# Performance work log

Hardware: AMD Instinct MI355X
Metric: run time of the kernel (lower is better)

The kernel has to match this reference:

```python
import jax, jax.numpy as jnp
import numpy as np

L, B, E, H = 4096, 4, 1024, 16
HD = E // H
EPS = 1e-4


def setup_inputs() -> dict:
    key = jax.random.key(0)
    ks = jax.random.split(key, 9)
    s = 1.0 / np.sqrt(E)
    return {
        "query": jax.random.normal(ks[0], (L, B, E), jnp.float32),
        "key_": jax.random.normal(ks[1], (L, B, E), jnp.float32),
        "value": jax.random.normal(ks[2], (L, B, E), jnp.float32),
        "Wq": jax.random.normal(ks[3], (E, E), jnp.float32) * s,
        "bq": jnp.zeros((E,), jnp.float32),
        "Wk": jax.random.normal(ks[4], (E, E), jnp.float32) * s,
        "bk": jnp.zeros((E,), jnp.float32),
        "Wv": jax.random.normal(ks[5], (E, E), jnp.float32) * s,
        "bv": jnp.zeros((E,), jnp.float32),
    }


def _heads(x):
    # (L, B, E) -> (B*H, L, HD)
    l = x.shape[0]
    return x.reshape(l, B * H, HD).transpose(1, 0, 2)


def reference(query, key_, value, Wq, bq, Wk, bk, Wv, bv):
    tgt_len = query.shape[0]
    src_len = key_.shape[0]
    q = _heads(query @ Wq.T + bq)
    k = _heads(key_ @ Wk.T + bk)
    v = _heads(value @ Wv.T + bv)
    # relu feature map (use_relu=True, constant=0)
    q = jax.nn.relu(q)
    k = jax.nn.relu(k)
    m = max(src_len, tgt_len)
    # pi/2 * arange(1, m+1) / m
    ang = (jnp.pi / 2) * jnp.arange(1, m + 1, dtype=q.dtype) / m  # (m,)
    sin = jnp.sin(ang)[None, :, None]
    cos = jnp.cos(ang)[None, :, None]
    q_ = jnp.concatenate([q * sin[:, :tgt_len], q * cos[:, :tgt_len]], axis=-1)  # (n, L, 2HD)
    k_ = jnp.concatenate([k * sin[:, :src_len], k * cos[:, :src_len]], axis=-1)
    # non-causal linear attention
    kv_ = jnp.einsum('nld,nlm->ndm', k_, v)                       # (n, 2HD, HD)
    z_ = 1.0 / jnp.maximum(jnp.einsum('nld,nd->nl', q_, k_.sum(axis=1)), EPS)
    attn = jnp.einsum('nld,ndm,nl->nlm', q_, kv_, z_)             # (n, L, HD)
    out = attn.transpose(1, 0, 2).reshape(tgt_len, B, E)
    return out
```

## Files before the change

### kernel.cpp

```cpp
#include <hip/hip_runtime.h>
#include <hip/hip_bf16.h>


typedef unsigned short ushortt;
typedef unsigned int u32;
typedef __attribute__((ext_vector_type(8))) short bf16x8;
typedef __attribute__((ext_vector_type(4))) float f32x4;

#define L_DIM 4096
#define B_DIM 4
#define E_DIM 1024

#define KV_CH 8
#define KV_LCH (L_DIM / KV_CH)
#define KV_LT 32

__device__ __forceinline__ ushortt f2bf(float f) {
    union { float f; u32 u; } v; v.f = f;
    u32 u = v.u;
    u += 0x7FFFu + ((u >> 16) & 1u);
    return (ushortt)(u >> 16);
}
__device__ __forceinline__ float bf2f(ushortt h) {
    union { u32 u; float f; } v; v.u = ((u32)h) << 16;
    return v.f;
}

__device__ __forceinline__ void gl_lds16(const void* g, void* l) {
    __builtin_amdgcn_global_load_lds(
        (const __attribute__((address_space(1))) unsigned int*)g,
        (__attribute__((address_space(3))) unsigned int*)l, 16, 0, 0);
}

__global__ __launch_bounds__(256) void k_cvtW(
    const float* __restrict__ W, ushortt* __restrict__ Wb)
{
    const int i = (blockIdx.x * 256 + threadIdx.x) * 4;
    const float4 v = *reinterpret_cast<const float4*>(W + i);
    ushortt o[4] = { f2bf(v.x), f2bf(v.y), f2bf(v.z), f2bf(v.w) };
    *reinterpret_cast<uint2*>(Wb + i) = *reinterpret_cast<uint2*>(o);
}

__global__ __launch_bounds__(256) void k_cvtX(
    const float* __restrict__ X, ushortt* __restrict__ Xb)
{
    const int i = (blockIdx.x * 256 + threadIdx.x) * 4;
    const float4 v = *reinterpret_cast<const float4*>(X + i);
    ushortt o[4] = { f2bf(v.x), f2bf(v.y), f2bf(v.z), f2bf(v.w) };
    *reinterpret_cast<uint2*>(Xb + i) = *reinterpret_cast<uint2*>(o);
}

__global__ __launch_bounds__(256) void k_gemmB(
    const ushortt* __restrict__ Xb, const ushortt* __restrict__ Wb,
    const float* __restrict__ bias,
    float* __restrict__ Of, ushortt* __restrict__ Ob, const int p)
{
    __shared__ char sA[2][8192];
    __shared__ char sB[2][8192];

    const int t = threadIdx.x;
    const int ln = t & 63;
    const int wv = t >> 6;
    const int wr = wv >> 1, wc = wv & 1;

    const int orig = blockIdx.x;
    const int bid = (orig & 7) * 128 + (orig >> 3);
    const int mblk = (bid >> 3) * 128;
    const int nblk = (bid & 7) * 128;

    f32x4 acc[4][4];
#pragma unroll
    for (int i = 0; i < 4; i++)
#pragma unroll
        for (int j = 0; j < 4; j++) acc[i][j] = (f32x4){0.f, 0.f, 0.f, 0.f};

    const int rowIn = ln >> 2;
    const int srcE  = ((ln & 3) ^ ((ln >> 3) & 3)) << 3;

    const int g   = ln >> 4;
    const int r15 = ln & 15;
    const int sw  = ((r15 >> 1) & 3) << 4;

    auto stage = [&](int buf, int k0) {
#pragma unroll
        for (int c = 0; c < 2; c++) {
            const int ch = wv * 2 + c;
            const int row = ch * 16 + rowIn;
            gl_lds16(Xb + (size_t)(mblk + row) * E_DIM + k0 + srcE, &sA[buf][ch * 1024]);
            gl_lds16(Wb + (size_t)(nblk + row) * E_DIM + k0 + srcE, &sB[buf][ch * 1024]);
        }
    };

    stage(0, 0);
    stage(1, 32);

    for (int tt = 0; tt < 32; tt++) {
        const int cur = tt & 1;
        if (tt < 31) {
            asm volatile("s_waitcnt vmcnt(4)" ::: "memory");
        } else {
            asm volatile("s_waitcnt vmcnt(0)" ::: "memory");
        }
        __builtin_amdgcn_sched_barrier(0);
        __builtin_amdgcn_s_barrier();

        bf16x8 va[4], vb[4];
#pragma unroll
        for (int i = 0; i < 4; i++) {
            const int row = wr * 64 + i * 16 + r15;
            va[i] = *reinterpret_cast<const bf16x8*>(&sA[cur][row * 64 + ((g * 16) ^ sw)]);
        }
#pragma unroll
        for (int j = 0; j < 4; j++) {
            const int n = wc * 64 + j * 16 + r15;
            vb[j] = *reinterpret_cast<const bf16x8*>(&sB[cur][n * 64 + ((g * 16) ^ sw)]);
        }
#pragma unroll
        for (int i = 0; i < 4; i++)
#pragma unroll
            for (int j = 0; j < 4; j++)
                acc[i][j] = __builtin_amdgcn_mfma_f32_16x16x32_bf16(va[i], vb[j], acc[i][j], 0, 0, 0);

        asm volatile("s_waitcnt lgkmcnt(0)" ::: "memory");
        __builtin_amdgcn_sched_barrier(0);
        __builtin_amdgcn_s_barrier();
        __builtin_amdgcn_sched_barrier(0);

        if (tt + 2 < 32) stage(cur, (tt + 2) * 32);
    }

#pragma unroll
    for (int j = 0; j < 4; j++) {
        const int col = nblk + wc * 64 + j * 16 + r15;
        const float bj = bias[col];
#pragma unroll
        for (int i = 0; i < 4; i++) {
            const int row0 = mblk + wr * 64 + i * 16 + g * 4;
#pragma unroll
            for (int r = 0; r < 4; r++) {
                float v = acc[i][j][r] + bj;
                if (p < 2) v = fmaxf(v, 0.0f);
                if (p == 0) Of[(size_t)(row0 + r) * E_DIM + col] = v;
                else        Ob[(size_t)(row0 + r) * E_DIM + col] = f2bf(v);
            }
        }
    }
}

__global__ __launch_bounds__(256) void k_kv3(
    const ushortt* __restrict__ Kb, const ushortt* __restrict__ Vb,
    float* __restrict__ pm, float* __restrict__ pd)
{
    __shared__ float sk[KV_LT][128];
    __shared__ float sv[KV_LT][64];

    const int head = blockIdx.x;
    const int b = head >> 4, hh = head & 15;
    const int t = threadIdx.x;
    const int mq = t & 7;
    const int dq = t >> 3;
    const int l0base = blockIdx.y * KV_LCH;

    float acc[4][8];
    float ksum[4];
#pragma unroll
    for (int i = 0; i < 4; i++) {
        ksum[i] = 0.0f;
#pragma unroll
        for (int j = 0; j < 8; j++) acc[i][j] = 0.0f;
    }

    const size_t headoff = (size_t)hh * 64;

    for (int l0 = l0base; l0 < l0base + KV_LCH; l0 += KV_LT) {
        __syncthreads();
#pragma unroll
        for (int i = 0; i < 2; i++) {
            const int j = t + 256 * i;
            const int l = j >> 4;
            const int c4 = (j & 15) << 2;
            const size_t rowb = ((size_t)(l0 + l) * B_DIM + b) * E_DIM + headoff;
            const uint2 kraw = *reinterpret_cast<const uint2*>(Kb + rowb + c4);
            const uint2 vraw = *reinterpret_cast<const uint2*>(Vb + rowb + c4);
            const float ang = 1.5707963267948966f * (float)(l0 + l + 1) * (1.0f / 4096.0f);
            const float sn = sinf(ang), cs = cosf(ang);
            const float k0 = bf2f((ushortt)(kraw.x & 0xffffu));
            const float k1 = bf2f((ushortt)(kraw.x >> 16));
            const float k2 = bf2f((ushortt)(kraw.y & 0xffffu));
            const float k3 = bf2f((ushortt)(kraw.y >> 16));
            *reinterpret_cast<float4*>(&sk[l][c4]) =
                make_float4(sn * k0, sn * k1, sn * k2, sn * k3);
            *reinterpret_cast<float4*>(&sk[l][64 + c4]) =
                make_float4(cs * k0, cs * k1, cs * k2, cs * k3);
            *reinterpret_cast<float4*>(&sv[l][c4]) =
                make_float4(bf2f((ushortt)(vraw.x & 0xffffu)),
                            bf2f((ushortt)(vraw.x >> 16)),
                            bf2f((ushortt)(vraw.y & 0xffffu)),
                            bf2f((ushortt)(vraw.y >> 16)));
        }
        __syncthreads();
#pragma unroll 8
        for (int l = 0; l < KV_LT; l++) {
            const float4 a4 = *reinterpret_cast<const float4*>(&sk[l][dq << 2]);
            const float4 v0 = *reinterpret_cast<const float4*>(&sv[l][mq << 3]);
            const float4 v1 = *reinterpret_cast<const float4*>(&sv[l][(mq << 3) + 4]);
            const float av[4] = { a4.x, a4.y, a4.z, a4.w };
            const float vv[8] = { v0.x, v0.y, v0.z, v0.w, v1.x, v1.y, v1.z, v1.w };
#pragma unroll
            for (int i = 0; i < 4; i++) {
#pragma unroll
                for (int j = 0; j < 8; j++) acc[i][j] += av[i] * vv[j];
                ksum[i] += av[i];
            }
        }
    }

    float* dstm = pm + ((size_t)blockIdx.y * 64 + head) * 8192;
    float* dstd = pd + ((size_t)blockIdx.y * 64 + head) * 128;
    const int d0 = dq << 2, m0 = mq << 3;
#pragma unroll
    for (int i = 0; i < 4; i++) {
        *reinterpret_cast<float4*>(&dstm[(d0 + i) * 64 + m0]) =
            make_float4(acc[i][0], acc[i][1], acc[i][2], acc[i][3]);
        *reinterpret_cast<float4*>(&dstm[(d0 + i) * 64 + m0 + 4]) =
            make_float4(acc[i][4], acc[i][5], acc[i][6], acc[i][7]);
        if (mq == 0) dstd[d0 + i] = ksum[i];
    }
}

__global__ __launch_bounds__(256) void k_kvred(
    const float* __restrict__ pm, const float* __restrict__ pd,
    float* __restrict__ kvm, float* __restrict__ kvd)
{
    const int bid = blockIdx.x, t = threadIdx.x;
    if (bid < 512) {
        const int g = bid * 256 + t;
        const int head = g >> 11, r = g & 2047;
        float4 s = make_float4(0.f, 0.f, 0.f, 0.f);
#pragma unroll
        for (int c = 0; c < KV_CH; c++) {
            const float4 v = reinterpret_cast<const float4*>(pm)[((size_t)(c * 64 + head) << 11) + r];
            s.x += v.x; s.y += v.y; s.z += v.z; s.w += v.w;
        }
        reinterpret_cast<float4*>(kvm)[g] = s;
    } else {
#pragma unroll
        for (int it = 0; it < 8; it++) {
            const int idx = it * 256 + t;
            const int head = idx >> 5, r = idx & 31;
            float4 s = make_float4(0.f, 0.f, 0.f, 0.f);
#pragma unroll
            for (int c = 0; c < KV_CH; c++) {
                const float4 v = reinterpret_cast<const float4*>(pd)[((size_t)(c * 64 + head) << 5) + r];
                s.x += v.x; s.y += v.y; s.z += v.z; s.w += v.w;
            }
            reinterpret_cast<float4*>(kvd)[idx] = s;
        }
    }
}

__global__ __launch_bounds__(256) void k_attn3(
    float* qout, const float* __restrict__ kvm, const float* __restrict__ kvd)
{
    __shared__ float skv[128][64];
    __shared__ float skd[128];
    __shared__ float sq[64][132];

    const int t = threadIdx.x;
    const int head = blockIdx.x;
    const int b = head >> 4, hh = head & 15;
    const int l0 = blockIdx.y * 64;

    const float* kvh = kvm + (size_t)head * (128 * 64);

#pragma unroll
    for (int c = 0; c < 8; c++) {
        const int idx = t + 256 * c;
        const int d = idx >> 4, m4 = (idx & 15) << 2;
        *reinterpret_cast<float4*>(&skv[d][m4]) =
            *reinterpret_cast<const float4*>(kvh + d * 64 + m4);
    }
    if (t < 128) skd[t] = kvd[(size_t)head * 128 + t];

    const size_t qbase = ((size_t)l0 * B_DIM + b) * E_DIM + (size_t)hh * 64;
#pragma unroll
    for (int c = 0; c < 4; c++) {
        const int idx = t + 256 * c;
        const int l = idx >> 4, q4 = (idx & 15) << 2;
        const float4 v = *reinterpret_cast<const float4*>(
            qout + qbase + (size_t)l * (B_DIM * E_DIM) + q4);
        const float ang = 1.5707963267948966f * (float)(l0 + l + 1) * (1.0f / 4096.0f);
        const float sn = sinf(ang), cs = cosf(ang);
        *reinterpret_cast<float4*>(&sq[l][q4]) =
            make_float4(sn * v.x, sn * v.y, sn * v.z, sn * v.w);
        *reinterpret_cast<float4*>(&sq[l][64 + q4]) =
            make_float4(cs * v.x, cs * v.y, cs * v.z, cs * v.w);
    }
    __syncthreads();

    const int tx = t & 15, ty = t >> 4;
    const int r = ty * 4, m0 = tx * 4;

    float4 acc[4];
    float accd[4];
#pragma unroll
    for (int i = 0; i < 4; i++) {
        acc[i] = make_float4(0.f, 0.f, 0.f, 0.f);
        accd[i] = 0.f;
    }

#pragma unroll 4
    for (int d0 = 0; d0 < 128; d0 += 4) {
        const float4 kd4 = *reinterpret_cast<const float4*>(&skd[d0]);
        float4 qv[4];
#pragma unroll
        for (int i = 0; i < 4; i++)
            qv[i] = *reinterpret_cast<const float4*>(&sq[r + i][d0]);
#pragma unroll
        for (int dd = 0; dd < 4; dd++) {
            const float4 kvv = *reinterpret_cast<const float4*>(&skv[d0 + dd][m0]);
            const float kdv = (dd == 0) ? kd4.x : (dd == 1) ? kd4.y : (dd == 2) ? kd4.z : kd4.w;
#pragma unroll
            for (int i = 0; i < 4; i++) {
                const float qs = (dd == 0) ? qv[i].x : (dd == 1) ? qv[i].y
                               : (dd == 2) ? qv[i].z : qv[i].w;
                acc[i].x += qs * kvv.x;
                acc[i].y += qs * kvv.y;
                acc[i].z += qs * kvv.z;
                acc[i].w += qs * kvv.w;
                accd[i] += qs * kdv;
            }
        }
    }

#pragma unroll
    for (int i = 0; i < 4; i++) {
        const float z = 1.0f / fmaxf(accd[i], 1e-4f);
        float4 vo = make_float4(acc[i].x * z, acc[i].y * z, acc[i].z * z, acc[i].w * z);
        *reinterpret_cast<float4*>(
            qout + qbase + (size_t)(r + i) * (B_DIM * E_DIM) + m0) = vo;
    }
}

extern "C" void kernel_launch(void* const* d_in, const int* in_sizes, int n_in,
                              void* d_out, int out_size, void* d_ws, size_t ws_size,
                              hipStream_t stream) {
    (void)in_sizes; (void)n_in; (void)out_size; (void)ws_size;
    const float* xq = (const float*)d_in[0];
    const float* xk = (const float*)d_in[1];
    const float* xv = (const float*)d_in[2];
    const float* wq = (const float*)d_in[3];
    const float* bq = (const float*)d_in[4];
    const float* wk = (const float*)d_in[5];
    const float* bk = (const float*)d_in[6];
    const float* wv = (const float*)d_in[7];
    const float* bv = (const float*)d_in[8];
    float* out = (float*)d_out;

    char* ws = (char*)d_ws;
    ushortt* Kb  = (ushortt*)(ws);
    ushortt* Vb  = (ushortt*)(ws + 33554432);
    ushortt* Wb  = (ushortt*)(ws + 67108864);
    float*   kvm = (float*)(ws + 67108864);
    float*   kvd = (float*)(ws + 67108864 + 2097152);
    ushortt* Xqb = (ushortt*)(ws);
    ushortt* Wqb = (ushortt*)(ws + 33554432);

    ushortt* Xkb = (ushortt*)d_out;
    ushortt* Xvb = (ushortt*)((char*)d_out + 33554432);
    float*   pm  = (float*)d_out;
    float*   pd  = (float*)((char*)d_out + 16777216);

    dim3 blk(256);
    k_cvtW<<<dim3(1024), blk, 0, stream>>>(wk, Wb);
    k_cvtX<<<dim3(16384), blk, 0, stream>>>(xk, Xkb);
    k_gemmB<<<dim3(1024), blk, 0, stream>>>(Xkb, Wb, bk, (float*)nullptr, Kb, 1);
    k_cvtW<<<dim3(1024), blk, 0, stream>>>(wv, Wb);
    k_cvtX<<<dim3(16384), blk, 0, stream>>>(xv, Xvb);
    k_gemmB<<<dim3(1024), blk, 0, stream>>>(Xvb, Wb, bv, (float*)nullptr, Vb, 2);
    k_kv3<<<dim3(64, KV_CH), blk, 0, stream>>>(Kb, Vb, pm, pd);
    k_kvred<<<dim3(513), blk, 0, stream>>>(pm, pd, kvm, kvd);
    k_cvtW<<<dim3(1024), blk, 0, stream>>>(wq, Wqb);
    k_cvtX<<<dim3(16384), blk, 0, stream>>>(xq, Xqb);
    k_gemmB<<<dim3(1024), blk, 0, stream>>>(Xqb, Wqb, bq, out, (ushortt*)nullptr, 0);
    k_attn3<<<dim3(64, 64), blk, 0, stream>>>(out, kvm, kvd);
}
```

Measured before the change: 557.0 us.

## Enlarge projection GEMM tiles to 256x256 with 512 threads and K-step 64

Replaces the 128x128-tile, 256-thread bf16 MFMA GEMM with a 256x256-tile, 512-thread version that stages K in chunks of 64 and uses a new XOR swizzle for the 128-byte LDS rows. It also hoists the bias loads ahead of the main loop. Larger tiles raise arithmetic intensity and halve the K-loop barrier count, which should cut global and LDS traffic per FLOP. The costs are 128 KB of LDS per block, more accumulator registers, and only 256 blocks, which may underfill the GPU's compute units.

```diff
diff --git a/kernel.cpp b/kernel.cpp
--- a/kernel.cpp
+++ b/kernel.cpp
@@ -50,95 +50,103 @@
     *reinterpret_cast<uint2*>(Xb + i) = *reinterpret_cast<uint2*>(o);
 }
 
-__global__ __launch_bounds__(256) void k_gemmB(
+__global__ __launch_bounds__(512, 2) void k_gemm256(
     const ushortt* __restrict__ Xb, const ushortt* __restrict__ Wb,
     const float* __restrict__ bias,
     float* __restrict__ Of, ushortt* __restrict__ Ob, const int p)
 {
-    __shared__ char sA[2][8192];
-    __shared__ char sB[2][8192];
+    __shared__ __align__(16) char sA[2][32768];
+    __shared__ __align__(16) char sB[2][32768];
 
     const int t = threadIdx.x;
     const int ln = t & 63;
     const int wv = t >> 6;
-    const int wr = wv >> 1, wc = wv & 1;
+    const int wr = wv >> 2;
+    const int wc = wv & 3;
 
     const int orig = blockIdx.x;
-    const int bid = (orig & 7) * 128 + (orig >> 3);
-    const int mblk = (bid >> 3) * 128;
-    const int nblk = (bid & 7) * 128;
-
-    f32x4 acc[4][4];
-#pragma unroll
-    for (int i = 0; i < 4; i++)
+    const int bid = (orig & 7) * 32 + (orig >> 3);
+    const int mblk = (bid >> 2) * 256;
+    const int nblk = (bid & 3) * 256;
+
+    f32x4 acc[8][4];
+#pragma unroll
+    for (int i = 0; i < 8; i++)
 #pragma unroll
         for (int j = 0; j < 4; j++) acc[i][j] = (f32x4){0.f, 0.f, 0.f, 0.f};
 
-    const int rowIn = ln >> 2;
-    const int srcE  = ((ln & 3) ^ ((ln >> 3) & 3)) << 3;
+    const int rowIn = ln >> 3;
+    const int srcE  = ((ln & 7) ^ rowIn) << 3;
 
     const int g   = ln >> 4;
     const int r15 = ln & 15;
-    const int sw  = ((r15 >> 1) & 3) << 4;
+    const int sw3 = r15 & 7;
 
     auto stage = [&](int buf, int k0) {
 #pragma unroll
-        for (int c = 0; c < 2; c++) {
-            const int ch = wv * 2 + c;
-            const int row = ch * 16 + rowIn;
+        for (int c = 0; c < 4; c++) {
+            const int ch = wv * 4 + c;
+            const int row = ch * 8 + rowIn;
             gl_lds16(Xb + (size_t)(mblk + row) * E_DIM + k0 + srcE, &sA[buf][ch * 1024]);
             gl_lds16(Wb + (size_t)(nblk + row) * E_DIM + k0 + srcE, &sB[buf][ch * 1024]);
         }
     };
 
+    float bj[4];
+#pragma unroll
+    for (int j = 0; j < 4; j++)
+        bj[j] = bias[nblk + wc * 64 + j * 16 + r15];
+    __builtin_amdgcn_sched_barrier(0);
+
     stage(0, 0);
-    stage(1, 32);
-
-    for (int tt = 0; tt < 32; tt++) {
+    stage(1, 64);
+
+    for (int tt = 0; tt < 16; tt++) {
         const int cur = tt & 1;
-        if (tt < 31) {
-            asm volatile("s_waitcnt vmcnt(4)" ::: "memory");
+        if (tt < 15) {
+            asm volatile("s_waitcnt vmcnt(8)" ::: "memory");
         } else {
             asm volatile("s_waitcnt vmcnt(0)" ::: "memory");
         }
         __builtin_amdgcn_sched_barrier(0);
         __builtin_amdgcn_s_barrier();
 
-        bf16x8 va[4], vb[4];
-#pragma unroll
-        for (int i = 0; i < 4; i++) {
-            const int row = wr * 64 + i * 16 + r15;
-            va[i] = *reinterpret_cast<const bf16x8*>(&sA[cur][row * 64 + ((g * 16) ^ sw)]);
-        }
-#pragma unroll
-        for (int j = 0; j < 4; j++) {
-            const int n = wc * 64 + j * 16 + r15;
-            vb[j] = *reinterpret_cast<const bf16x8*>(&sB[cur][n * 64 + ((g * 16) ^ sw)]);
-        }
-#pragma unroll
-        for (int i = 0; i < 4; i++)
-#pragma unroll
-            for (int j = 0; j < 4; j++)
-                acc[i][j] = __builtin_amdgcn_mfma_f32_16x16x32_bf16(va[i], vb[j], acc[i][j], 0, 0, 0);
+#pragma unroll
+        for (int ks = 0; ks < 2; ks++) {
+            const int off = ((ks * 4 + g) ^ sw3) << 4;
+            bf16x8 vb[4];
+#pragma unroll
+            for (int j = 0; j < 4; j++) {
+                const int row = wc * 64 + j * 16 + r15;
+                vb[j] = *reinterpret_cast<const bf16x8*>(&sB[cur][row * 128 + off]);
+            }
+#pragma unroll
+            for (int i = 0; i < 8; i++) {
+                const int row = wr * 128 + i * 16 + r15;
+                bf16x8 va = *reinterpret_cast<const bf16x8*>(&sA[cur][row * 128 + off]);
+#pragma unroll
+                for (int j = 0; j < 4; j++)
+                    acc[i][j] = __builtin_amdgcn_mfma_f32_16x16x32_bf16(va, vb[j], acc[i][j], 0, 0, 0);
+            }
+        }
 
         asm volatile("s_waitcnt lgkmcnt(0)" ::: "memory");
         __builtin_amdgcn_sched_barrier(0);
         __builtin_amdgcn_s_barrier();
         __builtin_amdgcn_sched_barrier(0);
 
-        if (tt + 2 < 32) stage(cur, (tt + 2) * 32);
+        if (tt + 2 < 16) stage(cur, (tt + 2) * 64);
     }
 
 #pragma unroll
     for (int j = 0; j < 4; j++) {
         const int col = nblk + wc * 64 + j * 16 + r15;
-        const float bj = bias[col];
-#pragma unroll
-        for (int i = 0; i < 4; i++) {
-            const int row0 = mblk + wr * 64 + i * 16 + g * 4;
+#pragma unroll
+        for (int i = 0; i < 8; i++) {
+            const int row0 = mblk + wr * 128 + i * 16 + g * 4;
 #pragma unroll
             for (int r = 0; r < 4; r++) {
-                float v = acc[i][j][r] + bj;
+                float v = acc[i][j][r] + bj[j];
                 if (p < 2) v = fmaxf(v, 0.0f);
                 if (p == 0) Of[(size_t)(row0 + r) * E_DIM + col] = v;
                 else        Ob[(size_t)(row0 + r) * E_DIM + col] = f2bf(v);
@@ -374,14 +382,14 @@
     dim3 blk(256);
     k_cvtW<<<dim3(1024), blk, 0, stream>>>(wk, Wb);
     k_cvtX<<<dim3(16384), blk, 0, stream>>>(xk, Xkb);
-    k_gemmB<<<dim3(1024), blk, 0, stream>>>(Xkb, Wb, bk, (float*)nullptr, Kb, 1);
+    k_gemm256<<<dim3(256), dim3(512), 0, stream>>>(Xkb, Wb, bk, (float*)nullptr, Kb, 1);
     k_cvtW<<<dim3(1024), blk, 0, stream>>>(wv, Wb);
     k_cvtX<<<dim3(16384), blk, 0, stream>>>(xv, Xvb);
-    k_gemmB<<<dim3(1024), blk, 0, stream>>>(Xvb, Wb, bv, (float*)nullptr, Vb, 2);
+    k_gemm256<<<dim3(256), dim3(512), 0, stream>>>(Xvb, Wb, bv, (float*)nullptr, Vb, 2);
     k_kv3<<<dim3(64, KV_CH), blk, 0, stream>>>(Kb, Vb, pm, pd);
     k_kvred<<<dim3(513), blk, 0, stream>>>(pm, pd, kvm, kvd);
     k_cvtW<<<dim3(1024), blk, 0, stream>>>(wq, Wqb);
     k_cvtX<<<dim3(16384), blk, 0, stream>>>(xq, Xqb);
-    k_gemmB<<<dim3(1024), blk, 0, stream>>>(Xqb, Wqb, bq, out, (ushortt*)nullptr, 0);
+    k_gemm256<<<dim3(256), dim3(512), 0, stream>>>(Xqb, Wqb, bq, out, (ushortt*)nullptr, 0);
     k_attn3<<<dim3(64, 64), blk, 0, stream>>>(out, kvm, kvd);
 }
```

Result: faster. 525.7 us (-5.6%).
